# Optimization experiments

Measured on AMD Instinct MI355X. Metric: run time of the kernel, lower is better.

## Reference

```python
import jax, jax.numpy as jnp
import numpy as np
import math

D_MODEL = 1024
NUM_HEAD = 16
D_HEAD = D_MODEL // NUM_HEAD
SEQ = 2048
BATCH = 2


def setup_inputs() -> dict:
    key = jax.random.key(0)
    k1, k2, k3, k4, k5 = jax.random.split(key, 5)
    s = 1.0 / math.sqrt(D_MODEL)
    return {
        "x": jax.random.normal(k1, (SEQ, BATCH, D_MODEL), dtype=jnp.float32),
        "qkv_w": jax.random.normal(k2, (3 * D_MODEL, D_MODEL), dtype=jnp.float32) * s,
        "qkv_b": jax.random.normal(k3, (3 * D_MODEL,), dtype=jnp.float32) * 0.01,
        "out_w": jax.random.normal(k4, (D_MODEL, D_MODEL), dtype=jnp.float32) * s,
        "out_b": jax.random.normal(k5, (D_MODEL,), dtype=jnp.float32) * 0.01,
        "is_causal": 1,
    }


def reference(x, qkv_w, qkv_b, out_w, out_b, is_causal):
    t, b, _ = x.shape
    qkv = x @ qkv_w.T + qkv_b  # [t, b, 3*d_model]
    # 't b (k h d) -> b k h t d'
    qkv = qkv.reshape(t, b, 3, NUM_HEAD, D_HEAD).transpose(1, 2, 3, 0, 4)
    q, k, v = qkv[:, 0], qkv[:, 1], qkv[:, 2]  # each [b, h, t, d]
    softmax_scale = 1.0 / math.sqrt(D_HEAD)
    # NOTE: faithful to source bug: score is DIVIDED by softmax_scale
    score = jnp.einsum('bhtd,bhsd->bhts', q, k) / softmax_scale
    if is_causal:
        causal_mask = jnp.triu(jnp.full((t, t), -1000000.0, dtype=score.dtype), k=1)
        score = score + causal_mask
    attn = jax.nn.softmax(score, axis=-1)
    av = jnp.einsum('bhts,bhsd->bhtd', attn, v)  # [b, h, t, d]
    av = av.transpose(2, 0, 1, 3).reshape(t, b, D_MODEL)  # 'b h t d -> t b (h d)'
    return av @ out_w.T + out_b
```

## Files before the change

kernel.cpp:

```cpp
#include <hip/hip_runtime.h>
#include <math.h>

#define TSEQ   2048
#define BB     2
#define DMODEL 1024
#define NHEAD  16
#define DHEAD  64
#define MROWS  (TSEQ * BB)
#define NQB    (TSEQ / 64)

typedef __attribute__((ext_vector_type(8))) _Float16 half8;
typedef __attribute__((ext_vector_type(4))) float    floatx4;
typedef unsigned short u16;
typedef unsigned int   u32;

#define QSCL 11.5415603f
#define MSK  1442695.0f

__device__ __forceinline__ u16 f2h(float f) {
    union { _Float16 h; u16 u; } cv;
    cv.h = (_Float16)f;
    return cv.u;
}

__device__ __forceinline__ u32 pkrtz(float a, float b) {
    typedef __attribute__((ext_vector_type(2))) __fp16 fp16x2;
    union { fp16x2 h; u32 u; } cv;
    cv.h = __builtin_amdgcn_cvt_pkrtz(a, b);
    return cv.u;
}

__device__ __forceinline__ void async_cp16(const u16* g, u16* l) {
    __builtin_amdgcn_global_load_lds(
        (const __attribute__((address_space(1))) unsigned int*)g,
        (__attribute__((address_space(3))) unsigned int*)l, 16, 0, 0);
}

__global__ __launch_bounds__(256)
void cast3_f32_f16(const float* __restrict__ a, u16* __restrict__ oa,
                   const float* __restrict__ b, u16* __restrict__ ob,
                   const float* __restrict__ c, u16* __restrict__ oc)
{
    int i = blockIdx.x * 256 + threadIdx.x;
    const float* src; u16* dst; int off;
    if (i < 1048576)      { src = a; dst = oa; off = 0; }
    else if (i < 1835008) { src = b; dst = ob; off = 1048576; }
    else                  { src = c; dst = oc; off = 1835008; }
    int j = i - off;
    float4 v = ((const float4*)src)[j];
    ushort4 o;
    o.x = f2h(v.x); o.y = f2h(v.y); o.z = f2h(v.z); o.w = f2h(v.w);
    ((ushort4*)dst)[j] = o;
}

__global__ __launch_bounds__(256)
void gemm_qkv(const u16* __restrict__ A, const u16* __restrict__ W,
              const float* __restrict__ bias,
              u16* __restrict__ Qo, u16* __restrict__ Ko, u16* __restrict__ Vo,
              int M, int N, int K)
{
    __shared__ __align__(16) u16 As[128][64];
    __shared__ __align__(16) u16 Bs[64][64];

    const int tid  = threadIdx.x;
    const int lane = tid & 63;
    const int wv   = tid >> 6;
    const int ln   = lane & 15, lh = lane >> 4;
    const int m0   = blockIdx.y * 128;
    const int n0   = blockIdx.x * 64;

    const int c = n0 >> 10;
    const bool vmode = (c == 2);

    const int srowA = wv * 32 + (lane >> 3);
    const int srowW = wv * 16 + (lane >> 3);
    const int sslot = lane & 7;

    const floatx4 zero4 = {0.0f, 0.0f, 0.0f, 0.0f};
    floatx4 acc[2][4];
#pragma unroll
    for (int i = 0; i < 2; ++i)
#pragma unroll
        for (int j = 0; j < 4; ++j) acc[i][j] = zero4;

    for (int k0 = 0; k0 < K; k0 += 64) {
        __syncthreads();
#pragma unroll
        for (int t = 0; t < 4; ++t) {
            const int row = srowA + t * 8;
            const int g   = sslot ^ (row & 7);
            async_cp16(A + (size_t)(m0 + row) * K + k0 + g * 8, &As[row][sslot * 8]);
        }
#pragma unroll
        for (int t = 0; t < 2; ++t) {
            const int row = srowW + t * 8;
            const int g   = sslot ^ (row & 7);
            async_cp16(W + (size_t)(n0 + row) * K + k0 + g * 8, &Bs[row][sslot * 8]);
        }
        __syncthreads();

#pragma unroll
        for (int ks = 0; ks < 2; ++ks) {
            half8 xf[2], wf[4];
#pragma unroll
            for (int i = 0; i < 2; ++i) {
                const int row = wv * 32 + i * 16 + ln;
                xf[i] = *(const half8*)&As[row][(((ks << 2) | lh) ^ (row & 7)) * 8];
            }
#pragma unroll
            for (int j = 0; j < 4; ++j) {
                const int row = j * 16 + ln;
                wf[j] = *(const half8*)&Bs[row][(((ks << 2) | lh) ^ (row & 7)) * 8];
            }
            if (vmode) {
#pragma unroll
                for (int i = 0; i < 2; ++i)
#pragma unroll
                    for (int j = 0; j < 4; ++j)
                        acc[i][j] = __builtin_amdgcn_mfma_f32_16x16x32_f16(xf[i], wf[j], acc[i][j], 0, 0, 0);
            } else {
#pragma unroll
                for (int i = 0; i < 2; ++i)
#pragma unroll
                    for (int j = 0; j < 4; ++j)
                        acc[i][j] = __builtin_amdgcn_mfma_f32_16x16x32_f16(wf[j], xf[i], acc[i][j], 0, 0, 0);
            }
        }
    }

    if (!vmode) {
        const float scl = (c == 0) ? QSCL : 1.0f;
        u16* dst = (c == 0) ? Qo : Ko;
#pragma unroll
        for (int j = 0; j < 4; ++j) {
            const int nb = n0 + j * 16 + lh * 4;
            const float4 b4 = *(const float4*)&bias[nb];
            const int h  = (nb >> 6) & 15;
            const int d0 = nb & 63;
#pragma unroll
            for (int i = 0; i < 2; ++i) {
                const int tok = m0 + wv * 32 + i * 16 + ln;
                const int t = tok >> 1, b = tok & 1;
                uint2 pk;
                pk.x = pkrtz((acc[i][j][0] + b4.x) * scl, (acc[i][j][1] + b4.y) * scl);
                pk.y = pkrtz((acc[i][j][2] + b4.z) * scl, (acc[i][j][3] + b4.w) * scl);
                *(uint2*)&dst[(((size_t)b * NHEAD + h) * TSEQ + t) * DHEAD + d0] = pk;
            }
        }
    } else {
#pragma unroll
        for (int j = 0; j < 4; ++j) {
            const int col = n0 + j * 16 + ln;
            const float bc = bias[col];
            const int h = (col >> 6) & 15;
            const int d = col & 63;
#pragma unroll
            for (int i = 0; i < 2; ++i) {
                const int mb = m0 + wv * 32 + i * 16 + lh * 4;
                const int t0 = mb >> 1;
                const u32 e0 = pkrtz(acc[i][j][0] + bc, acc[i][j][2] + bc);
                const u32 e1 = pkrtz(acc[i][j][1] + bc, acc[i][j][3] + bc);
                *(u32*)&Vo[(((size_t)0 * NHEAD + h) * DHEAD + d) * TSEQ + t0] = e0;
                *(u32*)&Vo[(((size_t)1 * NHEAD + h) * DHEAD + d) * TSEQ + t0] = e1;
            }
        }
    }
}

__global__ __launch_bounds__(256)
void gemm_out64(const u16* __restrict__ A, const u16* __restrict__ W,
                const float* __restrict__ bias, float* __restrict__ Cout,
                int M, int N, int K)
{
    __shared__ __align__(16) u16 As[64][64];
    __shared__ __align__(16) u16 Bs[64][64];

    const int tid  = threadIdx.x;
    const int lane = tid & 63;
    const int wv   = tid >> 6;
    const int ln   = lane & 15, lh = lane >> 4;
    const int m0   = blockIdx.y * 64;
    const int n0   = blockIdx.x * 64;

    const floatx4 zero4 = {0.0f, 0.0f, 0.0f, 0.0f};
    floatx4 acc[4];
#pragma unroll
    for (int j = 0; j < 4; ++j) acc[j] = zero4;

    for (int k0 = 0; k0 < K; k0 += 64) {
        __syncthreads();
#pragma unroll
        for (int cb = 0; cb < 2; ++cb) {
            const int idx  = cb * 256 + tid;
            const int row  = idx >> 3;
            const int slot = idx & 7;
            const int g    = slot ^ (row & 7);
            async_cp16(A + (size_t)(m0 + row) * K + k0 + g * 8, &As[row][slot * 8]);
            async_cp16(W + (size_t)(n0 + row) * K + k0 + g * 8, &Bs[row][slot * 8]);
        }
        __syncthreads();

#pragma unroll
        for (int ks = 0; ks < 2; ++ks) {
            const int arow = wv * 16 + ln;
            half8 xf = *(const half8*)&As[arow][(((ks << 2) | lh) ^ (arow & 7)) * 8];
#pragma unroll
            for (int j = 0; j < 4; ++j) {
                const int row = j * 16 + ln;
                half8 wf = *(const half8*)&Bs[row][(((ks << 2) | lh) ^ (row & 7)) * 8];
                acc[j] = __builtin_amdgcn_mfma_f32_16x16x32_f16(wf, xf, acc[j], 0, 0, 0);
            }
        }
    }

#pragma unroll
    for (int j = 0; j < 4; ++j) {
        const int fb = n0 + j * 16 + lh * 4;
        const float4 b4 = *(const float4*)&bias[fb];
        const int tok = m0 + wv * 16 + ln;
        float4 v;
        v.x = acc[j][0] + b4.x;
        v.y = acc[j][1] + b4.y;
        v.z = acc[j][2] + b4.z;
        v.w = acc[j][3] + b4.w;
        *(float4*)&Cout[(size_t)tok * N + fb] = v;
    }
}

__global__ __launch_bounds__(256)
void flash_f16(const u16* __restrict__ Q, const u16* __restrict__ K,
               const u16* __restrict__ Vt, u16* __restrict__ AV,
               const int* __restrict__ causal_p)
{
    __shared__ __align__(16) u16 smem[(64 + 64 + 80) * 72];
    u16 (* __restrict__ QPs)[72] = (u16(*)[72])smem;
    u16 (* __restrict__ Ks)[72]  = (u16(*)[72])(smem + 64 * 72);
    u16 (* __restrict__ Vs)[72]  = (u16(*)[72])(smem + 128 * 72);

    const int tid  = threadIdx.x;
    const int lane = tid & 63;
    const int wv   = tid >> 6;
    const int ln   = lane & 15, lh = lane >> 4;

    const int phase = blockIdx.x >> 8;
    const int slot  = blockIdx.x & 255;
    const int bh    = slot & 31;
    const int jq    = slot >> 5;
    int qb;
    if      (phase == 0) qb = 31 - jq;
    else if (phase == 1) qb = jq;
    else if (phase == 2) qb = 23 - jq;
    else                 qb = 8 + jq;

    const int b = bh >> 4;
    const int h = bh & 15;
    const int causal = causal_p[0];

    const u16* Qg = Q  + (size_t)bh * TSEQ * DHEAD;
    const u16* Kg = K  + (size_t)bh * TSEQ * DHEAD;
    const u16* Vg = Vt + (size_t)bh * DHEAD * TSEQ;

    const int lrow = tid >> 3;
    const int lc8  = (tid & 7) * 8;

    *(uint4*)&QPs[lrow][lc8]      = *(const uint4*)(Qg + (size_t)(qb * 64 + lrow) * DHEAD + lc8);
    *(uint4*)&QPs[lrow + 32][lc8] = *(const uint4*)(Qg + (size_t)(qb * 64 + lrow + 32) * DHEAD + lc8);
    for (int idx = tid; idx < 16 * 72; idx += 256) {
        const int rr = idx / 72, cc = idx % 72;
        Vs[64 + rr][cc] = (rr == 0) ? (u16)0x3C00 : (u16)0;
    }
    uint4 kreg0 = *(const uint4*)(Kg + (size_t)lrow * DHEAD + lc8);
    uint4 kreg1 = *(const uint4*)(Kg + (size_t)(lrow + 32) * DHEAD + lc8);
    uint4 vreg0 = *(const uint4*)(Vg + (size_t)lrow * TSEQ + lc8);
    uint4 vreg1 = *(const uint4*)(Vg + (size_t)(lrow + 32) * TSEQ + lc8);
    __syncthreads();

    const int qr0  = wv * 16;
    const int qloc = qr0 + ln;
    const half8 bQ0 = *(const half8*)&QPs[qloc][lh * 8];
    const half8 bQ1 = *(const half8*)&QPs[qloc][32 + lh * 8];
    const half8 bO0 = *(const half8*)&Vs[64 + ln][lh * 8];
    const half8 bO1 = *(const half8*)&Vs[64 + ln][32 + lh * 8];

    const floatx4 zero4 = {0.0f, 0.0f, 0.0f, 0.0f};
    floatx4 o[4], o4;
#pragma unroll
    for (int j = 0; j < 4; ++j) o[j] = zero4;
    o4 = zero4;
    float m_i = -3.0e38f;

    const int kb_end = causal ? qb : (TSEQ / 64 - 1);
    for (int kb = 0; kb <= kb_end; ++kb) {
        *(uint4*)&Ks[lrow][lc8]      = kreg0;
        *(uint4*)&Ks[lrow + 32][lc8] = kreg1;
        *(uint4*)&Vs[lrow][lc8]      = vreg0;
        *(uint4*)&Vs[lrow + 32][lc8] = vreg1;
        __syncthreads();

        if (kb < kb_end) {
            const size_t nk = (size_t)(kb + 1) * 64;
            kreg0 = *(const uint4*)(Kg + (nk + lrow) * DHEAD + lc8);
            kreg1 = *(const uint4*)(Kg + (nk + lrow + 32) * DHEAD + lc8);
            vreg0 = *(const uint4*)(Vg + (size_t)lrow * TSEQ + nk + lc8);
            vreg1 = *(const uint4*)(Vg + (size_t)(lrow + 32) * TSEQ + nk + lc8);
        }

        floatx4 s[4];
#pragma unroll
        for (int j = 0; j < 4; ++j) {
            half8 aK0 = *(const half8*)&Ks[j * 16 + ln][lh * 8];
            half8 aK1 = *(const half8*)&Ks[j * 16 + ln][32 + lh * 8];
            floatx4 z = zero4;
            z = __builtin_amdgcn_mfma_f32_16x16x32_f16(aK0, bQ0, z, 0, 0, 0);
            z = __builtin_amdgcn_mfma_f32_16x16x32_f16(aK1, bQ1, z, 0, 0, 0);
            s[j] = z;
        }
        if ((causal != 0) && (kb == qb)) {
#pragma unroll
            for (int j = 0; j < 4; ++j)
#pragma unroll
                for (int r = 0; r < 4; ++r)
                    if (j * 16 + lh * 4 + r > qloc) s[j][r] -= MSK;
        }

        float mx = m_i;
#pragma unroll
        for (int j = 0; j < 4; ++j)
#pragma unroll
            for (int r = 0; r < 4; ++r) mx = fmaxf(mx, s[j][r]);
        mx = fmaxf(mx, __shfl_xor(mx, 16));
        mx = fmaxf(mx, __shfl_xor(mx, 32));
        const float alpha = exp2f(m_i - mx);
        m_i = mx;

#pragma unroll
        for (int j = 0; j < 4; ++j) {
            uint2 pk;
            pk.x = pkrtz(exp2f(s[j][0] - mx), exp2f(s[j][1] - mx));
            pk.y = pkrtz(exp2f(s[j][2] - mx), exp2f(s[j][3] - mx));
            *(uint2*)&QPs[qloc][j * 16 + lh * 4] = pk;
        }

        float a_r[4];
#pragma unroll
        for (int r = 0; r < 4; ++r) a_r[r] = __shfl(alpha, lh * 4 + r);
#pragma unroll
        for (int j = 0; j < 4; ++j)
#pragma unroll
            for (int r = 0; r < 4; ++r) o[j][r] *= a_r[r];
#pragma unroll
        for (int r = 0; r < 4; ++r) o4[r] *= a_r[r];

        half8 aP0 = *(const half8*)&QPs[qloc][lh * 8];
        half8 aP1 = *(const half8*)&QPs[qloc][32 + lh * 8];
#pragma unroll
        for (int j = 0; j < 4; ++j) {
            half8 bV0 = *(const half8*)&Vs[j * 16 + ln][lh * 8];
            half8 bV1 = *(const half8*)&Vs[j * 16 + ln][32 + lh * 8];
            o[j] = __builtin_amdgcn_mfma_f32_16x16x32_f16(aP0, bV0, o[j], 0, 0, 0);
            o[j] = __builtin_amdgcn_mfma_f32_16x16x32_f16(aP1, bV1, o[j], 0, 0, 0);
        }
        o4 = __builtin_amdgcn_mfma_f32_16x16x32_f16(aP0, bO0, o4, 0, 0, 0);
        o4 = __builtin_amdgcn_mfma_f32_16x16x32_f16(aP1, bO1, o4, 0, 0, 0);

        __syncthreads();
    }

#pragma unroll
    for (int r = 0; r < 4; ++r) {
        const float lr = __shfl(o4[r], lane & 48);
        const float il = 1.0f / lr;
        const int qrow = qb * 64 + qr0 + lh * 4 + r;
#pragma unroll
        for (int j = 0; j < 4; ++j) {
            const int d = j * 16 + ln;
            AV[((size_t)qrow * BB + b) * DMODEL + h * 64 + d] = f2h(o[j][r] * il);
        }
    }
}

extern "C" void kernel_launch(void* const* d_in, const int* in_sizes, int n_in,
                              void* d_out, int out_size, void* d_ws, size_t ws_size,
                              hipStream_t stream)
{
    const float* x      = (const float*)d_in[0];
    const float* qkv_w  = (const float*)d_in[1];
    const float* qkv_b  = (const float*)d_in[2];
    const float* out_w  = (const float*)d_in[3];
    const float* out_b  = (const float*)d_in[4];
    const int*   is_causal = (const int*)d_in[5];
    float* out = (float*)d_out;

    u16* ws   = (u16*)d_ws;
    u16* xb   = ws;
    u16* wqkv = xb   + (size_t)4194304;
    u16* wout = wqkv + (size_t)3145728;
    u16* Qh   = wout + (size_t)1048576;
    u16* Kh   = Qh   + (size_t)4194304;
    u16* Vth  = Kh   + (size_t)4194304;
    u16* AVh  = Vth  + (size_t)4194304;

    cast3_f32_f16<<<8192, 256, 0, stream>>>(x, xb, qkv_w, wqkv, out_w, wout);

    gemm_qkv<<<dim3(3 * DMODEL / 64, MROWS / 128), 256, 0, stream>>>(
        xb, wqkv, qkv_b, Qh, Kh, Vth, MROWS, 3 * DMODEL, DMODEL);

    flash_f16<<<1024, 256, 0, stream>>>(Qh, Kh, Vth, AVh, is_causal);

    gemm_out64<<<dim3(DMODEL / 64, MROWS / 64), 256, 0, stream>>>(
        AVh, wout, out_b, out, MROWS, DMODEL, DMODEL);
}
```

Measured before the change: 195.9 us.

## Restructure flash attention to register-resident K/V fragments with two query tiles per wave

The flash kernel now uses 128 threads per block, and each wave handles two 16-row query tiles. K and V fragments are loaded straight from global memory into registers (K prefetched one block ahead), which removes the shared K/V staging and the block-wide barriers. A lazy rescale skips the accumulator correction unless the running max grows by more than a threshold. The block index mapping is also changed to group heads differently. The cost is higher register pressure and redundant, less coalesced global loads of V per wave, which now rely on the cache.

```diff
diff --git a/kernel.cpp b/kernel.cpp
--- a/kernel.cpp
+++ b/kernel.cpp
@@ -7,7 +7,6 @@
 #define NHEAD  16
 #define DHEAD  64
 #define MROWS  (TSEQ * BB)
-#define NQB    (TSEQ / 64)
 
 typedef __attribute__((ext_vector_type(8))) _Float16 half8;
 typedef __attribute__((ext_vector_type(4))) float    floatx4;
@@ -227,155 +226,212 @@
     }
 }
 
-__global__ __launch_bounds__(256)
+__global__ __launch_bounds__(128, 2)
 void flash_f16(const u16* __restrict__ Q, const u16* __restrict__ K,
                const u16* __restrict__ Vt, u16* __restrict__ AV,
                const int* __restrict__ causal_p)
 {
-    __shared__ __align__(16) u16 smem[(64 + 64 + 80) * 72];
-    u16 (* __restrict__ QPs)[72] = (u16(*)[72])smem;
-    u16 (* __restrict__ Ks)[72]  = (u16(*)[72])(smem + 64 * 72);
-    u16 (* __restrict__ Vs)[72]  = (u16(*)[72])(smem + 128 * 72);
+    __shared__ __align__(16) u16 Ps[64][72];
 
     const int tid  = threadIdx.x;
     const int lane = tid & 63;
     const int wv   = tid >> 6;
     const int ln   = lane & 15, lh = lane >> 4;
 
-    const int phase = blockIdx.x >> 8;
-    const int slot  = blockIdx.x & 255;
-    const int bh    = slot & 31;
-    const int jq    = slot >> 5;
+    const int bid  = blockIdx.x;
+    const int bh   = ((bid >> 3) & 3) * 8 + (bid & 7);
+    const int rest = bid >> 5;
+    const int ph   = rest >> 3, jq = rest & 7;
     int qb;
-    if      (phase == 0) qb = 31 - jq;
-    else if (phase == 1) qb = jq;
-    else if (phase == 2) qb = 23 - jq;
-    else                 qb = 8 + jq;
-
-    const int b = bh >> 4;
-    const int h = bh & 15;
+    if      (ph == 0) qb = 31 - jq;
+    else if (ph == 1) qb = jq;
+    else if (ph == 2) qb = 23 - jq;
+    else              qb = 8 + jq;
+
+    const int b = bh >> 4, h = bh & 15;
     const int causal = causal_p[0];
 
     const u16* Qg = Q  + (size_t)bh * TSEQ * DHEAD;
     const u16* Kg = K  + (size_t)bh * TSEQ * DHEAD;
     const u16* Vg = Vt + (size_t)bh * DHEAD * TSEQ;
 
-    const int lrow = tid >> 3;
-    const int lc8  = (tid & 7) * 8;
-
-    *(uint4*)&QPs[lrow][lc8]      = *(const uint4*)(Qg + (size_t)(qb * 64 + lrow) * DHEAD + lc8);
-    *(uint4*)&QPs[lrow + 32][lc8] = *(const uint4*)(Qg + (size_t)(qb * 64 + lrow + 32) * DHEAD + lc8);
-    for (int idx = tid; idx < 16 * 72; idx += 256) {
-        const int rr = idx / 72, cc = idx % 72;
-        Vs[64 + rr][cc] = (rr == 0) ? (u16)0x3C00 : (u16)0;
-    }
-    uint4 kreg0 = *(const uint4*)(Kg + (size_t)lrow * DHEAD + lc8);
-    uint4 kreg1 = *(const uint4*)(Kg + (size_t)(lrow + 32) * DHEAD + lc8);
-    uint4 vreg0 = *(const uint4*)(Vg + (size_t)lrow * TSEQ + lc8);
-    uint4 vreg1 = *(const uint4*)(Vg + (size_t)(lrow + 32) * TSEQ + lc8);
-    __syncthreads();
-
-    const int qr0  = wv * 16;
-    const int qloc = qr0 + ln;
-    const half8 bQ0 = *(const half8*)&QPs[qloc][lh * 8];
-    const half8 bQ1 = *(const half8*)&QPs[qloc][32 + lh * 8];
-    const half8 bO0 = *(const half8*)&Vs[64 + ln][lh * 8];
-    const half8 bO1 = *(const half8*)&Vs[64 + ln][32 + lh * 8];
+    const int G0 = qb * 64 + wv * 32;
+    const int G1 = G0 + 16;
+
+    const half8 q00 = *(const half8*)(Qg + (size_t)(G0 + ln) * DHEAD + lh * 8);
+    const half8 q01 = *(const half8*)(Qg + (size_t)(G0 + ln) * DHEAD + 32 + lh * 8);
+    const half8 q10 = *(const half8*)(Qg + (size_t)(G1 + ln) * DHEAD + lh * 8);
+    const half8 q11 = *(const half8*)(Qg + (size_t)(G1 + ln) * DHEAD + 32 + lh * 8);
+
+    const _Float16 ov = (_Float16)((ln == 0) ? 1.0f : 0.0f);
+    const half8 ones = {ov, ov, ov, ov, ov, ov, ov, ov};
 
     const floatx4 zero4 = {0.0f, 0.0f, 0.0f, 0.0f};
-    floatx4 o[4], o4;
-#pragma unroll
-    for (int j = 0; j < 4; ++j) o[j] = zero4;
-    o4 = zero4;
-    float m_i = -3.0e38f;
+    floatx4 o0[4], o1[4], o40, o41;
+#pragma unroll
+    for (int j = 0; j < 4; ++j) { o0[j] = zero4; o1[j] = zero4; }
+    o40 = zero4; o41 = zero4;
+    float m0 = -3.0e38f, m1 = -3.0e38f;
 
     const int kb_end = causal ? qb : (TSEQ / 64 - 1);
+
+    half8 kf[8];
+#pragma unroll
+    for (int j = 0; j < 4; ++j) {
+        const u16* kr = Kg + (size_t)(j * 16 + ln) * DHEAD + lh * 8;
+        kf[2 * j]     = *(const half8*)(kr);
+        kf[2 * j + 1] = *(const half8*)(kr + 32);
+    }
+
     for (int kb = 0; kb <= kb_end; ++kb) {
-        *(uint4*)&Ks[lrow][lc8]      = kreg0;
-        *(uint4*)&Ks[lrow + 32][lc8] = kreg1;
-        *(uint4*)&Vs[lrow][lc8]      = vreg0;
-        *(uint4*)&Vs[lrow + 32][lc8] = vreg1;
-        __syncthreads();
-
+        floatx4 s0[4], s1[4];
+#pragma unroll
+        for (int j = 0; j < 4; ++j) {
+            floatx4 z = zero4;
+            z = __builtin_amdgcn_mfma_f32_16x16x32_f16(kf[2 * j],     q00, z, 0, 0, 0);
+            z = __builtin_amdgcn_mfma_f32_16x16x32_f16(kf[2 * j + 1], q01, z, 0, 0, 0);
+            s0[j] = z;
+        }
+#pragma unroll
+        for (int j = 0; j < 4; ++j) {
+            floatx4 z = zero4;
+            z = __builtin_amdgcn_mfma_f32_16x16x32_f16(kf[2 * j],     q10, z, 0, 0, 0);
+            z = __builtin_amdgcn_mfma_f32_16x16x32_f16(kf[2 * j + 1], q11, z, 0, 0, 0);
+            s1[j] = z;
+        }
+
+        half8 vf[8];
+        {
+            const u16* vp = Vg + kb * 64;
+#pragma unroll
+            for (int j = 0; j < 4; ++j) {
+                const u16* vr = vp + (size_t)(j * 16 + ln) * TSEQ + lh * 8;
+                vf[2 * j]     = *(const half8*)(vr);
+                vf[2 * j + 1] = *(const half8*)(vr + 32);
+            }
+        }
+
+        half8 kfn[8];
         if (kb < kb_end) {
-            const size_t nk = (size_t)(kb + 1) * 64;
-            kreg0 = *(const uint4*)(Kg + (nk + lrow) * DHEAD + lc8);
-            kreg1 = *(const uint4*)(Kg + (nk + lrow + 32) * DHEAD + lc8);
-            vreg0 = *(const uint4*)(Vg + (size_t)lrow * TSEQ + nk + lc8);
-            vreg1 = *(const uint4*)(Vg + (size_t)(lrow + 32) * TSEQ + nk + lc8);
-        }
-
-        floatx4 s[4];
-#pragma unroll
-        for (int j = 0; j < 4; ++j) {
-            half8 aK0 = *(const half8*)&Ks[j * 16 + ln][lh * 8];
-            half8 aK1 = *(const half8*)&Ks[j * 16 + ln][32 + lh * 8];
-            floatx4 z = zero4;
-            z = __builtin_amdgcn_mfma_f32_16x16x32_f16(aK0, bQ0, z, 0, 0, 0);
-            z = __builtin_amdgcn_mfma_f32_16x16x32_f16(aK1, bQ1, z, 0, 0, 0);
-            s[j] = z;
-        }
-        if ((causal != 0) && (kb == qb)) {
+            const u16* kp = Kg + (size_t)(kb + 1) * 64 * DHEAD;
+#pragma unroll
+            for (int j = 0; j < 4; ++j) {
+                const u16* kr = kp + (size_t)(j * 16 + ln) * DHEAD + lh * 8;
+                kfn[2 * j]     = *(const half8*)(kr);
+                kfn[2 * j + 1] = *(const half8*)(kr + 32);
+            }
+        }
+
+        if (causal && kb == qb) {
 #pragma unroll
             for (int j = 0; j < 4; ++j)
 #pragma unroll
-                for (int r = 0; r < 4; ++r)
-                    if (j * 16 + lh * 4 + r > qloc) s[j][r] -= MSK;
-        }
-
-        float mx = m_i;
+                for (int r = 0; r < 4; ++r) {
+                    const int key = kb * 64 + j * 16 + lh * 4 + r;
+                    if (key > G0 + ln) s0[j][r] -= MSK;
+                    if (key > G1 + ln) s1[j][r] -= MSK;
+                }
+        }
+
+        {
+            float mx = m0;
+#pragma unroll
+            for (int j = 0; j < 4; ++j)
+#pragma unroll
+                for (int r = 0; r < 4; ++r) mx = fmaxf(mx, s0[j][r]);
+            mx = fmaxf(mx, __shfl_xor(mx, 16));
+            mx = fmaxf(mx, __shfl_xor(mx, 32));
+            if (!__all(mx <= m0 + 8.0f)) {
+                const float al = exp2f(m0 - mx);
+                m0 = mx;
+                float ar[4];
+#pragma unroll
+                for (int r = 0; r < 4; ++r) ar[r] = __shfl(al, lh * 4 + r);
+#pragma unroll
+                for (int j = 0; j < 4; ++j)
+#pragma unroll
+                    for (int r = 0; r < 4; ++r) o0[j][r] *= ar[r];
+#pragma unroll
+                for (int r = 0; r < 4; ++r) o40[r] *= ar[r];
+            }
+#pragma unroll
+            for (int j = 0; j < 4; ++j) {
+                uint2 pk;
+                pk.x = pkrtz(exp2f(s0[j][0] - m0), exp2f(s0[j][1] - m0));
+                pk.y = pkrtz(exp2f(s0[j][2] - m0), exp2f(s0[j][3] - m0));
+                *(uint2*)&Ps[wv * 32 + ln][j * 16 + lh * 4] = pk;
+            }
+        }
+
+        {
+            float mx = m1;
+#pragma unroll
+            for (int j = 0; j < 4; ++j)
+#pragma unroll
+                for (int r = 0; r < 4; ++r) mx = fmaxf(mx, s1[j][r]);
+            mx = fmaxf(mx, __shfl_xor(mx, 16));
+            mx = fmaxf(mx, __shfl_xor(mx, 32));
+            if (!__all(mx <= m1 + 8.0f)) {
+                const float al = exp2f(m1 - mx);
+                m1 = mx;
+                float ar[4];
+#pragma unroll
+                for (int r = 0; r < 4; ++r) ar[r] = __shfl(al, lh * 4 + r);
+#pragma unroll
+                for (int j = 0; j < 4; ++j)
+#pragma unroll
+                    for (int r = 0; r < 4; ++r) o1[j][r] *= ar[r];
+#pragma unroll
+                for (int r = 0; r < 4; ++r) o41[r] *= ar[r];
+            }
+#pragma unroll
+            for (int j = 0; j < 4; ++j) {
+                uint2 pk;
+                pk.x = pkrtz(exp2f(s1[j][0] - m1), exp2f(s1[j][1] - m1));
+                pk.y = pkrtz(exp2f(s1[j][2] - m1), exp2f(s1[j][3] - m1));
+                *(uint2*)&Ps[wv * 32 + 16 + ln][j * 16 + lh * 4] = pk;
+            }
+        }
+
+        {
+            const int r0 = wv * 32 + ln, r1 = r0 + 16;
+            half8 pa00 = *(const half8*)&Ps[r0][lh * 8];
+            half8 pa01 = *(const half8*)&Ps[r0][32 + lh * 8];
+            half8 pa10 = *(const half8*)&Ps[r1][lh * 8];
+            half8 pa11 = *(const half8*)&Ps[r1][32 + lh * 8];
+#pragma unroll
+            for (int j = 0; j < 4; ++j) {
+                o0[j] = __builtin_amdgcn_mfma_f32_16x16x32_f16(pa00, vf[2 * j],     o0[j], 0, 0, 0);
+                o0[j] = __builtin_amdgcn_mfma_f32_16x16x32_f16(pa01, vf[2 * j + 1], o0[j], 0, 0, 0);
+                o1[j] = __builtin_amdgcn_mfma_f32_16x16x32_f16(pa10, vf[2 * j],     o1[j], 0, 0, 0);
+                o1[j] = __builtin_amdgcn_mfma_f32_16x16x32_f16(pa11, vf[2 * j + 1], o1[j], 0, 0, 0);
+            }
+            o40 = __builtin_amdgcn_mfma_f32_16x16x32_f16(pa00, ones, o40, 0, 0, 0);
+            o40 = __builtin_amdgcn_mfma_f32_16x16x32_f16(pa01, ones, o40, 0, 0, 0);
+            o41 = __builtin_amdgcn_mfma_f32_16x16x32_f16(pa10, ones, o41, 0, 0, 0);
+            o41 = __builtin_amdgcn_mfma_f32_16x16x32_f16(pa11, ones, o41, 0, 0, 0);
+        }
+
+        if (kb < kb_end) {
+#pragma unroll
+            for (int i = 0; i < 8; ++i) kf[i] = kfn[i];
+        }
+    }
+
+#pragma unroll
+    for (int r = 0; r < 4; ++r) {
+        const float l0  = __shfl(o40[r], lane & 48);
+        const float il0 = 1.0f / l0;
+        const int   qr0 = G0 + lh * 4 + r;
 #pragma unroll
         for (int j = 0; j < 4; ++j)
-#pragma unroll
-            for (int r = 0; r < 4; ++r) mx = fmaxf(mx, s[j][r]);
-        mx = fmaxf(mx, __shfl_xor(mx, 16));
-        mx = fmaxf(mx, __shfl_xor(mx, 32));
-        const float alpha = exp2f(m_i - mx);
-        m_i = mx;
-
-#pragma unroll
-        for (int j = 0; j < 4; ++j) {
-            uint2 pk;
-            pk.x = pkrtz(exp2f(s[j][0] - mx), exp2f(s[j][1] - mx));
-            pk.y = pkrtz(exp2f(s[j][2] - mx), exp2f(s[j][3] - mx));
-            *(uint2*)&QPs[qloc][j * 16 + lh * 4] = pk;
-        }
-
-        float a_r[4];
-#pragma unroll
-        for (int r = 0; r < 4; ++r) a_r[r] = __shfl(alpha, lh * 4 + r);
+            AV[((size_t)qr0 * BB + b) * DMODEL + h * 64 + j * 16 + ln] = f2h(o0[j][r] * il0);
+        const float l1  = __shfl(o41[r], lane & 48);
+        const float il1 = 1.0f / l1;
+        const int   qr1 = G1 + lh * 4 + r;
 #pragma unroll
         for (int j = 0; j < 4; ++j)
-#pragma unroll
-            for (int r = 0; r < 4; ++r) o[j][r] *= a_r[r];
-#pragma unroll
-        for (int r = 0; r < 4; ++r) o4[r] *= a_r[r];
-
-        half8 aP0 = *(const half8*)&QPs[qloc][lh * 8];
-        half8 aP1 = *(const half8*)&QPs[qloc][32 + lh * 8];
-#pragma unroll
-        for (int j = 0; j < 4; ++j) {
-            half8 bV0 = *(const half8*)&Vs[j * 16 + ln][lh * 8];
-            half8 bV1 = *(const half8*)&Vs[j * 16 + ln][32 + lh * 8];
-            o[j] = __builtin_amdgcn_mfma_f32_16x16x32_f16(aP0, bV0, o[j], 0, 0, 0);
-            o[j] = __builtin_amdgcn_mfma_f32_16x16x32_f16(aP1, bV1, o[j], 0, 0, 0);
-        }
-        o4 = __builtin_amdgcn_mfma_f32_16x16x32_f16(aP0, bO0, o4, 0, 0, 0);
-        o4 = __builtin_amdgcn_mfma_f32_16x16x32_f16(aP1, bO1, o4, 0, 0, 0);
-
-        __syncthreads();
-    }
-
-#pragma unroll
-    for (int r = 0; r < 4; ++r) {
-        const float lr = __shfl(o4[r], lane & 48);
-        const float il = 1.0f / lr;
-        const int qrow = qb * 64 + qr0 + lh * 4 + r;
-#pragma unroll
-        for (int j = 0; j < 4; ++j) {
-            const int d = j * 16 + ln;
-            AV[((size_t)qrow * BB + b) * DMODEL + h * 64 + d] = f2h(o[j][r] * il);
-        }
+            AV[((size_t)qr1 * BB + b) * DMODEL + h * 64 + j * 16 + ln] = f2h(o1[j][r] * il1);
     }
 }
 
@@ -405,7 +461,7 @@
     gemm_qkv<<<dim3(3 * DMODEL / 64, MROWS / 128), 256, 0, stream>>>(
         xb, wqkv, qkv_b, Qh, Kh, Vth, MROWS, 3 * DMODEL, DMODEL);
 
-    flash_f16<<<1024, 256, 0, stream>>>(Qh, Kh, Vth, AVh, is_causal);
+    flash_f16<<<1024, 128, 0, stream>>>(Qh, Kh, Vth, AVh, is_causal);
 
     gemm_out64<<<dim3(DMODEL / 64, MROWS / 64), 256, 0, stream>>>(
         AVh, wout, out_b, out, MROWS, DMODEL, DMODEL);
```

Result: slower. 209.9 us (+7.2%).

## Load Q from global, use lazy softmax rescale, prefetch V fragments, add setprio

Applied to the files above, without the earlier changes.

Q fragments are now read straight from global into registers instead of being staged in shared memory, and the row-sum ones matrix is built in registers, which shrinks shared memory and removes the initial sync. The online softmax skips rescaling the accumulators unless the running max grows by more than 8 (in log2 units), saving exp and multiply work on most iterations. V fragments are loaded before the softmax math so LDS latency overlaps it. The MFMA sections are wrapped in s_setprio and launch bounds request 4 blocks per CU. Lazy rescaling risks fp16 overflow of P values up to 2^8, though that bound stays within fp16 range.

```diff
diff --git a/kernel.cpp b/kernel.cpp
--- a/kernel.cpp
+++ b/kernel.cpp
@@ -7,7 +7,6 @@
 #define NHEAD  16
 #define DHEAD  64
 #define MROWS  (TSEQ * BB)
-#define NQB    (TSEQ / 64)
 
 typedef __attribute__((ext_vector_type(8))) _Float16 half8;
 typedef __attribute__((ext_vector_type(4))) float    floatx4;
@@ -227,15 +226,15 @@
     }
 }
 
-__global__ __launch_bounds__(256)
+__global__ __launch_bounds__(256, 4)
 void flash_f16(const u16* __restrict__ Q, const u16* __restrict__ K,
                const u16* __restrict__ Vt, u16* __restrict__ AV,
                const int* __restrict__ causal_p)
 {
-    __shared__ __align__(16) u16 smem[(64 + 64 + 80) * 72];
-    u16 (* __restrict__ QPs)[72] = (u16(*)[72])smem;
-    u16 (* __restrict__ Ks)[72]  = (u16(*)[72])(smem + 64 * 72);
-    u16 (* __restrict__ Vs)[72]  = (u16(*)[72])(smem + 128 * 72);
+    __shared__ __align__(16) u16 smem[192 * 72];
+    u16 (* __restrict__ Ps)[72] = (u16(*)[72])smem;
+    u16 (* __restrict__ Ks)[72] = (u16(*)[72])(smem + 64 * 72);
+    u16 (* __restrict__ Vs)[72] = (u16(*)[72])(smem + 128 * 72);
 
     const int tid  = threadIdx.x;
     const int lane = tid & 63;
@@ -263,33 +262,30 @@
     const int lrow = tid >> 3;
     const int lc8  = (tid & 7) * 8;
 
-    *(uint4*)&QPs[lrow][lc8]      = *(const uint4*)(Qg + (size_t)(qb * 64 + lrow) * DHEAD + lc8);
-    *(uint4*)&QPs[lrow + 32][lc8] = *(const uint4*)(Qg + (size_t)(qb * 64 + lrow + 32) * DHEAD + lc8);
-    for (int idx = tid; idx < 16 * 72; idx += 256) {
-        const int rr = idx / 72, cc = idx % 72;
-        Vs[64 + rr][cc] = (rr == 0) ? (u16)0x3C00 : (u16)0;
-    }
+    const int qr0   = wv * 16;
+    const int qloc  = qr0 + ln;
+    const int qglob = qb * 64 + qloc;
+
+    const half8 bQ0 = *(const half8*)(Qg + (size_t)qglob * DHEAD + lh * 8);
+    const half8 bQ1 = *(const half8*)(Qg + (size_t)qglob * DHEAD + 32 + lh * 8);
+
+    const _Float16 ov = (_Float16)((ln == 0) ? 1.0f : 0.0f);
+    const half8 ones = {ov, ov, ov, ov, ov, ov, ov, ov};
+
+    const floatx4 zero4 = {0.0f, 0.0f, 0.0f, 0.0f};
+    floatx4 o[4], o4;
+#pragma unroll
+    for (int j = 0; j < 4; ++j) o[j] = zero4;
+    o4 = zero4;
+    float m_i = -3.0e38f;
+
+    const int kb_end = causal ? qb : (TSEQ / 64 - 1);
+
     uint4 kreg0 = *(const uint4*)(Kg + (size_t)lrow * DHEAD + lc8);
     uint4 kreg1 = *(const uint4*)(Kg + (size_t)(lrow + 32) * DHEAD + lc8);
     uint4 vreg0 = *(const uint4*)(Vg + (size_t)lrow * TSEQ + lc8);
     uint4 vreg1 = *(const uint4*)(Vg + (size_t)(lrow + 32) * TSEQ + lc8);
-    __syncthreads();
-
-    const int qr0  = wv * 16;
-    const int qloc = qr0 + ln;
-    const half8 bQ0 = *(const half8*)&QPs[qloc][lh * 8];
-    const half8 bQ1 = *(const half8*)&QPs[qloc][32 + lh * 8];
-    const half8 bO0 = *(const half8*)&Vs[64 + ln][lh * 8];
-    const half8 bO1 = *(const half8*)&Vs[64 + ln][32 + lh * 8];
-
-    const floatx4 zero4 = {0.0f, 0.0f, 0.0f, 0.0f};
-    floatx4 o[4], o4;
-#pragma unroll
-    for (int j = 0; j < 4; ++j) o[j] = zero4;
-    o4 = zero4;
-    float m_i = -3.0e38f;
-
-    const int kb_end = causal ? qb : (TSEQ / 64 - 1);
+
     for (int kb = 0; kb <= kb_end; ++kb) {
         *(uint4*)&Ks[lrow][lc8]      = kreg0;
         *(uint4*)&Ks[lrow + 32][lc8] = kreg1;
@@ -306,6 +302,7 @@
         }
 
         floatx4 s[4];
+        __builtin_amdgcn_s_setprio(1);
 #pragma unroll
         for (int j = 0; j < 4; ++j) {
             half8 aK0 = *(const half8*)&Ks[j * 16 + ln][lh * 8];
@@ -315,6 +312,15 @@
             z = __builtin_amdgcn_mfma_f32_16x16x32_f16(aK1, bQ1, z, 0, 0, 0);
             s[j] = z;
         }
+        __builtin_amdgcn_s_setprio(0);
+
+        half8 bV[8];
+#pragma unroll
+        for (int j = 0; j < 4; ++j) {
+            bV[2 * j]     = *(const half8*)&Vs[j * 16 + ln][lh * 8];
+            bV[2 * j + 1] = *(const half8*)&Vs[j * 16 + ln][32 + lh * 8];
+        }
+
         if ((causal != 0) && (kb == qb)) {
 #pragma unroll
             for (int j = 0; j < 4; ++j)
@@ -330,38 +336,40 @@
             for (int r = 0; r < 4; ++r) mx = fmaxf(mx, s[j][r]);
         mx = fmaxf(mx, __shfl_xor(mx, 16));
         mx = fmaxf(mx, __shfl_xor(mx, 32));
-        const float alpha = exp2f(m_i - mx);
-        m_i = mx;
+
+        if (!__all(mx <= m_i + 8.0f)) {
+            const float alpha = exp2f(m_i - mx);
+            m_i = mx;
+            float a_r[4];
+#pragma unroll
+            for (int r = 0; r < 4; ++r) a_r[r] = __shfl(alpha, lh * 4 + r);
+#pragma unroll
+            for (int j = 0; j < 4; ++j)
+#pragma unroll
+                for (int r = 0; r < 4; ++r) o[j][r] *= a_r[r];
+#pragma unroll
+            for (int r = 0; r < 4; ++r) o4[r] *= a_r[r];
+        }
 
 #pragma unroll
         for (int j = 0; j < 4; ++j) {
             uint2 pk;
-            pk.x = pkrtz(exp2f(s[j][0] - mx), exp2f(s[j][1] - mx));
-            pk.y = pkrtz(exp2f(s[j][2] - mx), exp2f(s[j][3] - mx));
-            *(uint2*)&QPs[qloc][j * 16 + lh * 4] = pk;
-        }
-
-        float a_r[4];
-#pragma unroll
-        for (int r = 0; r < 4; ++r) a_r[r] = __shfl(alpha, lh * 4 + r);
-#pragma unroll
-        for (int j = 0; j < 4; ++j)
-#pragma unroll
-            for (int r = 0; r < 4; ++r) o[j][r] *= a_r[r];
-#pragma unroll
-        for (int r = 0; r < 4; ++r) o4[r] *= a_r[r];
-
-        half8 aP0 = *(const half8*)&QPs[qloc][lh * 8];
-        half8 aP1 = *(const half8*)&QPs[qloc][32 + lh * 8];
-#pragma unroll
-        for (int j = 0; j < 4; ++j) {
-            half8 bV0 = *(const half8*)&Vs[j * 16 + ln][lh * 8];
-            half8 bV1 = *(const half8*)&Vs[j * 16 + ln][32 + lh * 8];
-            o[j] = __builtin_amdgcn_mfma_f32_16x16x32_f16(aP0, bV0, o[j], 0, 0, 0);
-            o[j] = __builtin_amdgcn_mfma_f32_16x16x32_f16(aP1, bV1, o[j], 0, 0, 0);
-        }
-        o4 = __builtin_amdgcn_mfma_f32_16x16x32_f16(aP0, bO0, o4, 0, 0, 0);
-        o4 = __builtin_amdgcn_mfma_f32_16x16x32_f16(aP1, bO1, o4, 0, 0, 0);
+            pk.x = pkrtz(exp2f(s[j][0] - m_i), exp2f(s[j][1] - m_i));
+            pk.y = pkrtz(exp2f(s[j][2] - m_i), exp2f(s[j][3] - m_i));
+            *(uint2*)&Ps[qloc][j * 16 + lh * 4] = pk;
+        }
+
+        half8 aP0 = *(const half8*)&Ps[qloc][lh * 8];
+        half8 aP1 = *(const half8*)&Ps[qloc][32 + lh * 8];
+        __builtin_amdgcn_s_setprio(1);
+#pragma unroll
+        for (int j = 0; j < 4; ++j) {
+            o[j] = __builtin_amdgcn_mfma_f32_16x16x32_f16(aP0, bV[2 * j],     o[j], 0, 0, 0);
+            o[j] = __builtin_amdgcn_mfma_f32_16x16x32_f16(aP1, bV[2 * j + 1], o[j], 0, 0, 0);
+        }
+        o4 = __builtin_amdgcn_mfma_f32_16x16x32_f16(aP0, ones, o4, 0, 0, 0);
+        o4 = __builtin_amdgcn_mfma_f32_16x16x32_f16(aP1, ones, o4, 0, 0, 0);
+        __builtin_amdgcn_s_setprio(0);
 
         __syncthreads();
     }
```

Measured after the change: 198.0 us. About the same (+1.1%).
